# Optimization experiments

Hardware: AMD Instinct MI355X
Metric: run time of the kernel (lower is better)

The kernel has to match this reference:

```python
import jax, jax.numpy as jnp
import numpy as np

B, S, D, H = 2, 2048, 1024, 16
DK = D // H


def setup_inputs() -> dict:
    key = jax.random.key(0)
    ks = jax.random.split(key, 7)
    x = jax.random.normal(ks[0], (B, S, D), dtype=jnp.float32)
    gamma = jax.random.normal(ks[1], (D,), dtype=jnp.float32)
    mask = jax.random.randint(ks[2], (B, S), 0, 2, dtype=jnp.int32)
    w_qkv_w = jax.random.normal(ks[3], (D, 3 * D), dtype=jnp.float32) / np.sqrt(D)
    w_qkv_b = jax.random.normal(ks[4], (3 * D,), dtype=jnp.float32) * 0.02
    w_o_w = jax.random.normal(ks[5], (D, D), dtype=jnp.float32) / np.sqrt(D)
    w_o_b = jax.random.normal(ks[6], (D,), dtype=jnp.float32) * 0.02
    return {"x": x, "gamma": gamma, "mask": mask, "w_qkv_w": w_qkv_w,
            "w_qkv_b": w_qkv_b, "w_o_w": w_o_w, "w_o_b": w_o_b}


def reference(x, gamma, mask, w_qkv_w, w_qkv_b, w_o_w, w_o_b):
    b, s, d = x.shape
    # QKV projection, then per-head interleaved chunk (matches torch view+chunk)
    qkv = x @ w_qkv_w + w_qkv_b                      # [B,S,3D]
    qkv = qkv.reshape(b, s, H, 3 * DK).transpose(0, 2, 1, 3)  # [B,H,S,3*dk]
    q, k, v = jnp.split(qkv, 3, axis=-1)             # each [B,H,S,dk]
    scale = 1.0 / np.sqrt(DK).astype(np.float32)
    scores = jnp.einsum('bhqd,bhkd->bhqk', q, k) * scale  # [B,H,S,S]
    m = mask[:, None, None, :]                       # 2D mask -> [B,1,1,S]
    scores = jnp.where(m == 0, -jnp.inf, scores)
    attn = jax.nn.softmax(scores, axis=-1)           # dropout p=0.0 -> identity
    out = jnp.einsum('bhqk,bhkd->bhqd', attn, v)     # [B,H,S,dk]
    out = out.transpose(0, 2, 1, 3).reshape(b, s, d) # [B,S,D]
    out = out @ w_o_w + w_o_b
    return (gamma + 1.0) * out
```

## Files before the change

kernel.cpp:

```cpp
#include <hip/hip_runtime.h>
#include <hip/hip_bf16.h>


using bf16 = __hip_bfloat16;
typedef __attribute__((ext_vector_type(8))) short bf16x8;
typedef __attribute__((ext_vector_type(4))) float f32x4;

#define QSCALE 0.18033688011112042f

static __device__ __forceinline__ f32x4 mfma_bf16(bf16x8 a, bf16x8 b, f32x4 c) {
    return __builtin_amdgcn_mfma_f32_16x16x32_bf16(a, b, c, 0, 0, 0);
}

static __device__ __forceinline__ void gld_lds16(const void* g, void* s) {
    __builtin_amdgcn_global_load_lds(
        (const __attribute__((address_space(1))) unsigned int*)g,
        (__attribute__((address_space(3))) unsigned int*)s,
        16, 0, 0);
}

static __device__ __forceinline__ unsigned int pk_bf16(float lo, float hi) {
    unsigned int ul = __builtin_bit_cast(unsigned int, lo) + 0x8000u;
    unsigned int uh = __builtin_bit_cast(unsigned int, hi) + 0x8000u;
    return __builtin_amdgcn_perm(uh, ul, 0x07060302u);
}

__global__ void prep_kernel(const float* __restrict__ x, bf16* __restrict__ xb,
                            const float* __restrict__ wqkv, bf16* __restrict__ wqkvT,
                            const float* __restrict__ wo, bf16* __restrict__ woT) {
    __shared__ float tile[32][33];
    int blk = blockIdx.x;
    if (blk < 4096) {
        int i = blk * 256 + threadIdx.x;
        float4 f = reinterpret_cast<const float4*>(x)[i];
        xb[4*i+0] = __float2bfloat16(f.x);
        xb[4*i+1] = __float2bfloat16(f.y);
        xb[4*i+2] = __float2bfloat16(f.z);
        xb[4*i+3] = __float2bfloat16(f.w);
        return;
    }
    int xo = threadIdx.x & 31, yo = threadIdx.x >> 5;
    if (blk < 7168) {
        int idx = blk - 4096;
        int c0 = (idx % 96) * 32, r0 = (idx / 96) * 32;
#pragma unroll
        for (int i = 0; i < 32; i += 8)
            tile[yo + i][xo] = wqkv[(size_t)(r0 + yo + i) * 3072 + c0 + xo];
        __syncthreads();
#pragma unroll
        for (int i = 0; i < 32; i += 8) {
            int c = c0 + yo + i;
            int hh = c / 192, rem = c - hh * 192;
            int which = rem >> 6, dk = rem & 63;
            int rowp = which * 1024 + hh * 64 + dk;
            float sc = (which == 0) ? QSCALE : 1.0f;
            wqkvT[(size_t)rowp * 1024 + r0 + xo] = __float2bfloat16(tile[xo][yo + i] * sc);
        }
    } else {
        int idx = blk - 7168;
        int c0 = (idx & 31) * 32, r0 = (idx >> 5) * 32;
#pragma unroll
        for (int i = 0; i < 32; i += 8)
            tile[yo + i][xo] = wo[(size_t)(r0 + yo + i) * 1024 + c0 + xo];
        __syncthreads();
#pragma unroll
        for (int i = 0; i < 32; i += 8)
            woT[(size_t)(c0 + yo + i) * 1024 + r0 + xo] = __float2bfloat16(tile[xo][yo + i]);
    }
}

__global__ void transpose_v_kernel(const bf16* __restrict__ in, bf16* __restrict__ out) {
    __shared__ bf16 t[64][72];
    const int bh = blockIdx.y, s0 = blockIdx.x * 64;
    const int r = threadIdx.x >> 2, c16 = (threadIdx.x & 3) * 16;
    const uint4* src = (const uint4*)(in + ((size_t)bh * 2048 + s0 + r) * 64 + c16);
    uint4 a0 = src[0], a1 = src[1];
    *(uint4*)&t[r][c16] = a0;
    *(uint4*)&t[r][c16 + 8] = a1;
    __syncthreads();
    bf16 tmp[16];
#pragma unroll
    for (int ii = 0; ii < 16; ++ii) {
        int i = c16 + ii;
        int a = i >> 5, rem = i & 31, q = rem >> 3, jj = rem & 7;
        int sp = a * 32 + q * 4 + (jj < 4 ? jj : 16 + jj - 4);
        tmp[ii] = t[sp][r];
    }
    uint4* dst = (uint4*)(out + ((size_t)bh * 64 + r) * 2048 + s0 + c16);
    dst[0] = ((uint4*)tmp)[0];
    dst[1] = ((uint4*)tmp)[1];
}

template <int EPI, int TM, int MINW>
__global__ __launch_bounds__(256, MINW)
void gemm_bt_kernel(const bf16* __restrict__ A, const bf16* __restrict__ Bt,
                    int M, int N, int K,
                    const float* __restrict__ bias, const float* __restrict__ gamma,
                    bf16* __restrict__ Qout, bf16* __restrict__ Kout, bf16* __restrict__ Vout,
                    float* __restrict__ Cout) {
    constexpr int MI = TM / 32;
    constexpr int CA = TM / 32;
    __shared__ __align__(16) bf16 As[TM * 64];
    __shared__ __align__(16) bf16 Bs[128 * 64];

    const int tid  = threadIdx.x;
    const int wave = tid >> 6, lane = tid & 63;
    const int quad = lane >> 4, l16 = lane & 15;
    const int wr = wave >> 1, wc = wave & 1;
    const int bm = blockIdx.y, bn = blockIdx.x;

    f32x4 acc[MI][4] = {};

    const int crow = lane >> 3;
    const int sblk = (lane & 7) ^ (crow & 7);
    const bf16* gA[CA]; const bf16* gB[4]; bf16* lA[CA]; bf16* lB[4];
#pragma unroll
    for (int c = 0; c < CA; ++c) {
        int ch = wave * CA + c;
        gA[c] = A + (size_t)(bm * TM + ch * 8 + crow) * K + sblk * 8;
        lA[c] = As + ch * 512 + lane * 8;
    }
#pragma unroll
    for (int c = 0; c < 4; ++c) {
        int ch = wave * 4 + c;
        gB[c] = Bt + (size_t)(bn * 128 + ch * 8 + crow) * K + sblk * 8;
        lB[c] = Bs + ch * 512 + lane * 8;
    }
    const int xr = l16 & 7;

    for (int k0 = 0; k0 < K; k0 += 64) {
#pragma unroll
        for (int c = 0; c < CA; ++c) gld_lds16(gA[c] + k0, lA[c]);
#pragma unroll
        for (int c = 0; c < 4; ++c) gld_lds16(gB[c] + k0, lB[c]);
        __syncthreads();
#pragma unroll
        for (int ks = 0; ks < 2; ++ks) {
            bf16x8 af[MI], bfr[4];
#pragma unroll
            for (int mi = 0; mi < MI; ++mi)
                af[mi] = *(const bf16x8*)(As + (wr * (TM/2) + mi * 16 + l16) * 64 + ((4 * ks + quad) ^ xr) * 8);
#pragma unroll
            for (int ni = 0; ni < 4; ++ni)
                bfr[ni] = *(const bf16x8*)(Bs + (wc * 64 + ni * 16 + l16) * 64 + ((4 * ks + quad) ^ xr) * 8);
#pragma unroll
            for (int mi = 0; mi < MI; ++mi)
#pragma unroll
                for (int ni = 0; ni < 4; ++ni)
                    acc[mi][ni] = mfma_bf16(af[mi], bfr[ni], acc[mi][ni]);
        }
        __syncthreads();
    }

#pragma unroll
    for (int mi = 0; mi < MI; ++mi) {
#pragma unroll
        for (int ni = 0; ni < 4; ++ni) {
            int col = bn * 128 + wc * 64 + ni * 16 + l16;
            if (EPI == 0) {
                int which = col >> 10, hh = (col >> 6) & 15, dk = col & 63;
                float bsc = (which == 0) ? QSCALE : 1.0f;
                float bv = bias[hh * 192 + which * 64 + dk] * bsc;
                bf16* dst = (which == 0) ? Qout : ((which == 1) ? Kout : Vout);
#pragma unroll
                for (int r = 0; r < 4; ++r) {
                    int row = bm * TM + wr * (TM/2) + mi * 16 + quad * 4 + r;
                    int b = row >> 11, s = row & 2047;
                    dst[(((size_t)b * 16 + hh) * 2048 + s) * 64 + dk] =
                        __float2bfloat16(acc[mi][ni][r] + bv);
                }
            } else {
                float g1 = gamma[col] + 1.0f, bv = bias[col];
#pragma unroll
                for (int r = 0; r < 4; ++r) {
                    int row = bm * TM + wr * (TM/2) + mi * 16 + quad * 4 + r;
                    Cout[(size_t)row * N + col] = g1 * (acc[mi][ni][r] + bv);
                }
            }
        }
    }
}

__global__ __launch_bounds__(256, 2)
void attn_kernel(const bf16* __restrict__ Qb, const bf16* __restrict__ Kb,
                 const bf16* __restrict__ Vtp, const int* __restrict__ mask,
                 bf16* __restrict__ Aout) {
    __shared__ __align__(16) unsigned char smem[66560];
    bf16* KsB = (bf16*)smem;
    bf16* VsB = (bf16*)(smem + 32768);
    float* BiasB = (float*)(smem + 65536);

    const int bh = blockIdx.y;
    const int b = bh >> 4, h = bh & 15;
    const int q0 = blockIdx.x * 128;
    const int tid = threadIdx.x;
    const int wave = tid >> 6, lane = tid & 63;
    const int quad = lane >> 4, l16 = lane & 15;
    const int xr = l16 & 7;
    const int qw = wave & 1, kh = wave >> 1;

    bf16x8 aq[4][2];
#pragma unroll
    for (int m = 0; m < 4; ++m) {
        const bf16* qp = Qb + ((size_t)bh * 2048 + q0 + qw * 64 + m * 16 + l16) * 64;
        aq[m][0] = *(const bf16x8*)(qp + quad * 8);
        aq[m][1] = *(const bf16x8*)(qp + 32 + quad * 8);
    }

    bf16x8 ones;
#pragma unroll
    for (int j = 0; j < 8; ++j) ones[j] = (short)0x3F80;

    f32x4 O[4][4] = {};
    f32x4 Lacc[4] = {};

    const int r8 = lane >> 3, b8 = lane & 7;
    const int srcb = b8 ^ r8;
    const bf16* gK = Kb  + ((size_t)bh * 2048 + kh * 1024 + qw * 8 + r8) * 64 + srcb * 8;
    const bf16* gV = Vtp + ((size_t)bh * 64 + qw * 8 + r8) * 2048 + kh * 1024 + srcb * 8;
    bf16* lK[2][4]; bf16* lV[2][4];
#pragma unroll
    for (int p = 0; p < 2; ++p)
#pragma unroll
        for (int c = 0; c < 4; ++c) {
            lK[p][c] = KsB + (kh * 2 + p) * 4096 + c * 1024 + qw * 512 + lane * 8;
            lV[p][c] = VsB + (kh * 2 + p) * 4096 + c * 1024 + qw * 512 + lane * 8;
        }

    int mreg = 0;
#pragma unroll
    for (int c = 0; c < 4; ++c) {
        gld_lds16(gK + c * 1024, lK[0][c]);
        gld_lds16(gV + (size_t)c * 32768, lV[0][c]);
    }
    if (qw == 0) {
        BiasB[(kh * 2) * 64 + lane] = mask[b * 2048 + kh * 1024 + lane] ? -24.0f : -1e30f;
        mreg = mask[b * 2048 + kh * 1024 + 64 + lane];
    }

    for (int kt = 0; kt < 16; ++kt) {
        __syncthreads();
        const int cur = kt & 1, nxt = cur ^ 1;

        if (kt + 1 < 16) {
#pragma unroll
            for (int c = 0; c < 4; ++c) {
                gld_lds16(gK + (size_t)(kt + 1) * 4096 + c * 1024, lK[nxt][c]);
                gld_lds16(gV + (kt + 1) * 64 + (size_t)c * 32768, lV[nxt][c]);
            }
            if (qw == 0) BiasB[(kh * 2 + nxt) * 64 + lane] = mreg ? -24.0f : -1e30f;
        }
        if (kt + 2 < 16 && qw == 0) mreg = mask[b * 2048 + kh * 1024 + (kt + 2) * 64 + lane];

        const bf16* Ksc = KsB + (kh * 2 + cur) * 4096;
        const bf16* Vsc = VsB + (kh * 2 + cur) * 4096;
        const float* Bic = BiasB + (kh * 2 + cur) * 64;

        f32x4 bias4[4];
        bf16x8 bk[4][2];
#pragma unroll
        for (int kt4 = 0; kt4 < 4; ++kt4) {
            bias4[kt4] = *(const f32x4*)(Bic + kt4 * 16 + quad * 4);
            const bf16* kp = Ksc + (kt4 * 16 + l16) * 64;
            bk[kt4][0] = *(const bf16x8*)(kp + (quad ^ xr) * 8);
            bk[kt4][1] = *(const bf16x8*)(kp + ((quad + 4) ^ xr) * 8);
        }
        bf16x8 bv8[2][4];
#pragma unroll
        for (int a = 0; a < 2; ++a)
#pragma unroll
            for (int nt = 0; nt < 4; ++nt)
                bv8[a][nt] = *(const bf16x8*)(Vsc + (nt * 16 + l16) * 64 + ((a * 4 + quad) ^ xr) * 8);

#pragma unroll
        for (int m = 0; m < 4; ++m) {
            f32x4 sv[4];
#pragma unroll
            for (int kt4 = 0; kt4 < 4; ++kt4) {
                f32x4 c = {0.f, 0.f, 0.f, 0.f};
                c = mfma_bf16(bk[kt4][0], aq[m][0], c);
                c = mfma_bf16(bk[kt4][1], aq[m][1], c);
                sv[kt4] = c;
            }
            float p[4][4];
#pragma unroll
            for (int kt4 = 0; kt4 < 4; ++kt4)
#pragma unroll
                for (int r = 0; r < 4; ++r)
                    p[kt4][r] = __builtin_amdgcn_exp2f(sv[kt4][r] + bias4[kt4][r]);

#pragma unroll
            for (int a = 0; a < 2; ++a) {
                uint4 uv;
                uv.x = pk_bf16(p[2*a][0],   p[2*a][1]);
                uv.y = pk_bf16(p[2*a][2],   p[2*a][3]);
                uv.z = pk_bf16(p[2*a+1][0], p[2*a+1][1]);
                uv.w = pk_bf16(p[2*a+1][2], p[2*a+1][3]);
                bf16x8 pa = __builtin_bit_cast(bf16x8, uv);
                Lacc[m] = mfma_bf16(pa, ones, Lacc[m]);
#pragma unroll
                for (int nt = 0; nt < 4; ++nt)
                    O[m][nt] = mfma_bf16(pa, bv8[a][nt], O[m][nt]);
            }
        }
    }

    __syncthreads();
    float* mg = (float*)smem;
    float* mp = mg + (qw * 64 + lane) * 81;
    if (kh == 1) {
#pragma unroll
        for (int m = 0; m < 4; ++m) {
#pragma unroll
            for (int nt = 0; nt < 4; ++nt)
#pragma unroll
                for (int r = 0; r < 4; ++r) mp[m * 16 + nt * 4 + r] = O[m][nt][r];
#pragma unroll
            for (int r = 0; r < 4; ++r) mp[64 + m * 4 + r] = Lacc[m][r];
        }
    }
    __syncthreads();
    if (kh == 0) {
#pragma unroll
        for (int m = 0; m < 4; ++m) {
#pragma unroll
            for (int nt = 0; nt < 4; ++nt)
#pragma unroll
                for (int r = 0; r < 4; ++r) O[m][nt][r] += mp[m * 16 + nt * 4 + r];
#pragma unroll
            for (int r = 0; r < 4; ++r) Lacc[m][r] += mp[64 + m * 4 + r];
        }
#pragma unroll
        for (int m = 0; m < 4; ++m) {
            float inv[4];
#pragma unroll
            for (int r = 0; r < 4; ++r) inv[r] = __builtin_amdgcn_rcpf(Lacc[m][r]);
#pragma unroll
            for (int nt = 0; nt < 4; ++nt) {
#pragma unroll
                for (int r = 0; r < 4; ++r) {
                    int row = q0 + qw * 64 + m * 16 + quad * 4 + r;
                    Aout[((size_t)b * 2048 + row) * 1024 + h * 64 + nt * 16 + l16] =
                        __float2bfloat16(O[m][nt][r] * inv[r]);
                }
            }
        }
    }
}

extern "C" void kernel_launch(void* const* d_in, const int* in_sizes, int n_in,
                              void* d_out, int out_size, void* d_ws, size_t ws_size,
                              hipStream_t stream) {
    const float* x     = (const float*)d_in[0];
    const float* gamma = (const float*)d_in[1];
    const int*   mask  = (const int*)d_in[2];
    const float* wqkv  = (const float*)d_in[3];
    const float* bqkv  = (const float*)d_in[4];
    const float* wo    = (const float*)d_in[5];
    const float* bo    = (const float*)d_in[6];
    float* out = (float*)d_out;

    char* ws = (char*)d_ws;
    const size_t MB = 1u << 20;
    bf16* xb    = (bf16*)(ws);
    bf16* wqkvT = (bf16*)(ws + 8 * MB);
    bf16* woT   = (bf16*)(ws + 14 * MB);
    bf16* Qb    = (bf16*)(ws + 16 * MB);
    bf16* Kb    = (bf16*)(ws + 24 * MB);
    bf16* Vt    = (bf16*)(ws + 32 * MB);
    bf16* Vtmp  = (bf16*)(ws + 40 * MB);
    bf16* attn  = (bf16*)(ws + 40 * MB);

    prep_kernel<<<8192, 256, 0, stream>>>(x, xb, wqkv, wqkvT, wo, woT);

    gemm_bt_kernel<0, 128, 3><<<dim3(24, 32), 256, 0, stream>>>(
        xb, wqkvT, 4096, 3072, 1024, bqkv, nullptr, Qb, Kb, Vtmp, nullptr);

    transpose_v_kernel<<<dim3(32, 32), 256, 0, stream>>>(Vtmp, Vt);

    attn_kernel<<<dim3(16, 32), 256, 0, stream>>>(Qb, Kb, Vt, mask, attn);

    gemm_bt_kernel<1, 64, 4><<<dim3(8, 64), 256, 0, stream>>>(
        attn, woT, 4096, 1024, 1024, bo, gamma, nullptr, nullptr, nullptr, out);
}
```

Measured before the change: 200.1 us.

## Fuse V transpose into QKV GEMM epilogue and drop attention key-split

The QKV GEMM epilogue for V column blocks now stages results in shared memory and writes V already transposed in the permuted layout attention expects, removing the separate transpose kernel and its round trip through memory. The attention kernel is also reworked from 4 waves splitting keys into two halves to 2 waves that each walk all keys. This drops the cross-wave shared-memory reduction at the end, at the cost of halving threads per block and doubling the serial key loop length. The launch bounds change to 128 threads with one block per SM hint, which may reduce latency hiding.

```diff
diff --git a/kernel.cpp b/kernel.cpp
--- a/kernel.cpp
+++ b/kernel.cpp
@@ -69,28 +69,6 @@
     }
 }
 
-__global__ void transpose_v_kernel(const bf16* __restrict__ in, bf16* __restrict__ out) {
-    __shared__ bf16 t[64][72];
-    const int bh = blockIdx.y, s0 = blockIdx.x * 64;
-    const int r = threadIdx.x >> 2, c16 = (threadIdx.x & 3) * 16;
-    const uint4* src = (const uint4*)(in + ((size_t)bh * 2048 + s0 + r) * 64 + c16);
-    uint4 a0 = src[0], a1 = src[1];
-    *(uint4*)&t[r][c16] = a0;
-    *(uint4*)&t[r][c16 + 8] = a1;
-    __syncthreads();
-    bf16 tmp[16];
-#pragma unroll
-    for (int ii = 0; ii < 16; ++ii) {
-        int i = c16 + ii;
-        int a = i >> 5, rem = i & 31, q = rem >> 3, jj = rem & 7;
-        int sp = a * 32 + q * 4 + (jj < 4 ? jj : 16 + jj - 4);
-        tmp[ii] = t[sp][r];
-    }
-    uint4* dst = (uint4*)(out + ((size_t)bh * 64 + r) * 2048 + s0 + c16);
-    dst[0] = ((uint4*)tmp)[0];
-    dst[1] = ((uint4*)tmp)[1];
-}
-
 template <int EPI, int TM, int MINW>
 __global__ __launch_bounds__(256, MINW)
 void gemm_bt_kernel(const bf16* __restrict__ A, const bf16* __restrict__ Bt,
@@ -100,8 +78,9 @@
                     float* __restrict__ Cout) {
     constexpr int MI = TM / 32;
     constexpr int CA = TM / 32;
-    __shared__ __align__(16) bf16 As[TM * 64];
-    __shared__ __align__(16) bf16 Bs[128 * 64];
+    __shared__ __align__(16) bf16 smem[TM * 64 + 128 * 64];
+    bf16* As = smem;
+    bf16* Bs = smem + TM * 64;
 
     const int tid  = threadIdx.x;
     const int wave = tid >> 6, lane = tid & 63;
@@ -152,6 +131,41 @@
         __syncthreads();
     }
 
+    if (EPI == 0 && bn >= 16) {
+        __syncthreads();
+        uint2* Tu = (uint2*)smem;
+#pragma unroll
+        for (int mi = 0; mi < MI; ++mi) {
+#pragma unroll
+            for (int ni = 0; ni < 4; ++ni) {
+                int colL = wc * 64 + ni * 16 + l16;
+                float bv = bias[(2 * (bn - 16) + wc) * 192 + 128 + (ni * 16 + l16)];
+                uint2 pk;
+                pk.x = pk_bf16(acc[mi][ni][0] + bv, acc[mi][ni][1] + bv);
+                pk.y = pk_bf16(acc[mi][ni][2] + bv, acc[mi][ni][3] + bv);
+                int rg = wr * 16 + mi * 4 + quad;
+                Tu[colL * 32 + (rg ^ (colL & 31))] = pk;
+            }
+        }
+        __syncthreads();
+        const int sub = tid & 15, rbase = tid >> 4;
+        const int cs = sub >> 3, aa = (sub >> 2) & 1, qq = sub & 3;
+        const int g1 = cs * 16 + aa * 8 + qq;
+        const int g2 = g1 + 4;
+        const int b = bm >> 4;
+        const int s0 = (bm & 15) * 128;
+#pragma unroll
+        for (int j = 0; j < 8; ++j) {
+            int rt = rbase + 16 * j;
+            int hh = 2 * (bn - 16) + (rt >> 6), dk = rt & 63;
+            uint2 lo = Tu[rt * 32 + (g1 ^ (rt & 31))];
+            uint2 hi = Tu[rt * 32 + (g2 ^ (rt & 31))];
+            uint4 val; val.x = lo.x; val.y = lo.y; val.z = hi.x; val.w = hi.y;
+            *(uint4*)(Vout + (((size_t)b * 16 + hh) * 64 + dk) * 2048 + s0 + sub * 8) = val;
+        }
+        return;
+    }
+
 #pragma unroll
     for (int mi = 0; mi < MI; ++mi) {
 #pragma unroll
@@ -159,9 +173,9 @@
             int col = bn * 128 + wc * 64 + ni * 16 + l16;
             if (EPI == 0) {
                 int which = col >> 10, hh = (col >> 6) & 15, dk = col & 63;
-                float bsc = (which == 0) ? QSCALE : 1.0f;
-                float bv = bias[hh * 192 + which * 64 + dk] * bsc;
-                bf16* dst = (which == 0) ? Qout : ((which == 1) ? Kout : Vout);
+                float bv = bias[hh * 192 + which * 64 + dk];
+                if (which == 0) bv *= QSCALE;
+                bf16* dst = which ? Kout : Qout;
 #pragma unroll
                 for (int r = 0; r < 4; ++r) {
                     int row = bm * TM + wr * (TM/2) + mi * 16 + quad * 4 + r;
@@ -181,14 +195,13 @@
     }
 }
 
-__global__ __launch_bounds__(256, 2)
+__global__ __launch_bounds__(128, 1)
 void attn_kernel(const bf16* __restrict__ Qb, const bf16* __restrict__ Kb,
                  const bf16* __restrict__ Vtp, const int* __restrict__ mask,
                  bf16* __restrict__ Aout) {
-    __shared__ __align__(16) unsigned char smem[66560];
-    bf16* KsB = (bf16*)smem;
-    bf16* VsB = (bf16*)(smem + 32768);
-    float* BiasB = (float*)(smem + 65536);
+    __shared__ __align__(16) bf16 Ks[2][64 * 64];
+    __shared__ __align__(16) bf16 Vs[2][64 * 64];
+    __shared__ float Biass[2][64];
 
     const int bh = blockIdx.y;
     const int b = bh >> 4, h = bh & 15;
@@ -197,12 +210,11 @@
     const int wave = tid >> 6, lane = tid & 63;
     const int quad = lane >> 4, l16 = lane & 15;
     const int xr = l16 & 7;
-    const int qw = wave & 1, kh = wave >> 1;
 
     bf16x8 aq[4][2];
 #pragma unroll
     for (int m = 0; m < 4; ++m) {
-        const bf16* qp = Qb + ((size_t)bh * 2048 + q0 + qw * 64 + m * 16 + l16) * 64;
+        const bf16* qp = Qb + ((size_t)bh * 2048 + q0 + wave * 64 + m * 16 + l16) * 64;
         aq[m][0] = *(const bf16x8*)(qp + quad * 8);
         aq[m][1] = *(const bf16x8*)(qp + 32 + quad * 8);
     }
@@ -216,15 +228,15 @@
 
     const int r8 = lane >> 3, b8 = lane & 7;
     const int srcb = b8 ^ r8;
-    const bf16* gK = Kb  + ((size_t)bh * 2048 + kh * 1024 + qw * 8 + r8) * 64 + srcb * 8;
-    const bf16* gV = Vtp + ((size_t)bh * 64 + qw * 8 + r8) * 2048 + kh * 1024 + srcb * 8;
+    const bf16* gK = Kb  + ((size_t)bh * 2048 + wave * 8 + r8) * 64 + srcb * 8;
+    const bf16* gV = Vtp + ((size_t)bh * 64 + wave * 8 + r8) * 2048 + srcb * 8;
     bf16* lK[2][4]; bf16* lV[2][4];
 #pragma unroll
     for (int p = 0; p < 2; ++p)
 #pragma unroll
         for (int c = 0; c < 4; ++c) {
-            lK[p][c] = KsB + (kh * 2 + p) * 4096 + c * 1024 + qw * 512 + lane * 8;
-            lV[p][c] = VsB + (kh * 2 + p) * 4096 + c * 1024 + qw * 512 + lane * 8;
+            lK[p][c] = Ks[p] + c * 1024 + wave * 512 + lane * 8;
+            lV[p][c] = Vs[p] + c * 1024 + wave * 512 + lane * 8;
         }
 
     int mreg = 0;
@@ -233,35 +245,31 @@
         gld_lds16(gK + c * 1024, lK[0][c]);
         gld_lds16(gV + (size_t)c * 32768, lV[0][c]);
     }
-    if (qw == 0) {
-        BiasB[(kh * 2) * 64 + lane] = mask[b * 2048 + kh * 1024 + lane] ? -24.0f : -1e30f;
-        mreg = mask[b * 2048 + kh * 1024 + 64 + lane];
-    }
-
-    for (int kt = 0; kt < 16; ++kt) {
+    if (tid < 64) {
+        Biass[0][tid] = mask[b * 2048 + tid] ? -24.0f : -1e30f;
+        mreg = mask[b * 2048 + 64 + tid];
+    }
+
+    for (int kt = 0; kt < 32; ++kt) {
         __syncthreads();
         const int cur = kt & 1, nxt = cur ^ 1;
 
-        if (kt + 1 < 16) {
+        if (kt + 1 < 32) {
 #pragma unroll
             for (int c = 0; c < 4; ++c) {
                 gld_lds16(gK + (size_t)(kt + 1) * 4096 + c * 1024, lK[nxt][c]);
                 gld_lds16(gV + (kt + 1) * 64 + (size_t)c * 32768, lV[nxt][c]);
             }
-            if (qw == 0) BiasB[(kh * 2 + nxt) * 64 + lane] = mreg ? -24.0f : -1e30f;
-        }
-        if (kt + 2 < 16 && qw == 0) mreg = mask[b * 2048 + kh * 1024 + (kt + 2) * 64 + lane];
-
-        const bf16* Ksc = KsB + (kh * 2 + cur) * 4096;
-        const bf16* Vsc = VsB + (kh * 2 + cur) * 4096;
-        const float* Bic = BiasB + (kh * 2 + cur) * 64;
+            if (tid < 64) Biass[nxt][tid] = mreg ? -24.0f : -1e30f;
+        }
+        if (kt + 2 < 32 && tid < 64) mreg = mask[b * 2048 + (kt + 2) * 64 + tid];
 
         f32x4 bias4[4];
         bf16x8 bk[4][2];
 #pragma unroll
         for (int kt4 = 0; kt4 < 4; ++kt4) {
-            bias4[kt4] = *(const f32x4*)(Bic + kt4 * 16 + quad * 4);
-            const bf16* kp = Ksc + (kt4 * 16 + l16) * 64;
+            bias4[kt4] = *(const f32x4*)(&Biass[cur][0] + kt4 * 16 + quad * 4);
+            const bf16* kp = Ks[cur] + (kt4 * 16 + l16) * 64;
             bk[kt4][0] = *(const bf16x8*)(kp + (quad ^ xr) * 8);
             bk[kt4][1] = *(const bf16x8*)(kp + ((quad + 4) ^ xr) * 8);
         }
@@ -270,7 +278,7 @@
         for (int a = 0; a < 2; ++a)
 #pragma unroll
             for (int nt = 0; nt < 4; ++nt)
-                bv8[a][nt] = *(const bf16x8*)(Vsc + (nt * 16 + l16) * 64 + ((a * 4 + quad) ^ xr) * 8);
+                bv8[a][nt] = *(const bf16x8*)(Vs[cur] + (nt * 16 + l16) * 64 + ((a * 4 + quad) ^ xr) * 8);
 
 #pragma unroll
         for (int m = 0; m < 4; ++m) {
@@ -305,44 +313,18 @@
         }
     }
 
-    __syncthreads();
-    float* mg = (float*)smem;
-    float* mp = mg + (qw * 64 + lane) * 81;
-    if (kh == 1) {
-#pragma unroll
-        for (int m = 0; m < 4; ++m) {
-#pragma unroll
-            for (int nt = 0; nt < 4; ++nt)
-#pragma unroll
-                for (int r = 0; r < 4; ++r) mp[m * 16 + nt * 4 + r] = O[m][nt][r];
-#pragma unroll
-            for (int r = 0; r < 4; ++r) mp[64 + m * 4 + r] = Lacc[m][r];
-        }
-    }
-    __syncthreads();
-    if (kh == 0) {
-#pragma unroll
-        for (int m = 0; m < 4; ++m) {
-#pragma unroll
-            for (int nt = 0; nt < 4; ++nt)
-#pragma unroll
-                for (int r = 0; r < 4; ++r) O[m][nt][r] += mp[m * 16 + nt * 4 + r];
-#pragma unroll
-            for (int r = 0; r < 4; ++r) Lacc[m][r] += mp[64 + m * 4 + r];
-        }
-#pragma unroll
-        for (int m = 0; m < 4; ++m) {
-            float inv[4];
-#pragma unroll
-            for (int r = 0; r < 4; ++r) inv[r] = __builtin_amdgcn_rcpf(Lacc[m][r]);
-#pragma unroll
-            for (int nt = 0; nt < 4; ++nt) {
-#pragma unroll
-                for (int r = 0; r < 4; ++r) {
-                    int row = q0 + qw * 64 + m * 16 + quad * 4 + r;
-                    Aout[((size_t)b * 2048 + row) * 1024 + h * 64 + nt * 16 + l16] =
-                        __float2bfloat16(O[m][nt][r] * inv[r]);
-                }
+#pragma unroll
+    for (int m = 0; m < 4; ++m) {
+        float inv[4];
+#pragma unroll
+        for (int r = 0; r < 4; ++r) inv[r] = __builtin_amdgcn_rcpf(Lacc[m][r]);
+#pragma unroll
+        for (int nt = 0; nt < 4; ++nt) {
+#pragma unroll
+            for (int r = 0; r < 4; ++r) {
+                int row = q0 + wave * 64 + m * 16 + quad * 4 + r;
+                Aout[((size_t)b * 2048 + row) * 1024 + h * 64 + nt * 16 + l16] =
+                    __float2bfloat16(O[m][nt][r] * inv[r]);
             }
         }
     }
@@ -368,17 +350,14 @@
     bf16* Qb    = (bf16*)(ws + 16 * MB);
     bf16* Kb    = (bf16*)(ws + 24 * MB);
     bf16* Vt    = (bf16*)(ws + 32 * MB);
-    bf16* Vtmp  = (bf16*)(ws + 40 * MB);
     bf16* attn  = (bf16*)(ws + 40 * MB);
 
     prep_kernel<<<8192, 256, 0, stream>>>(x, xb, wqkv, wqkvT, wo, woT);
 
     gemm_bt_kernel<0, 128, 3><<<dim3(24, 32), 256, 0, stream>>>(
-        xb, wqkvT, 4096, 3072, 1024, bqkv, nullptr, Qb, Kb, Vtmp, nullptr);
-
-    transpose_v_kernel<<<dim3(32, 32), 256, 0, stream>>>(Vtmp, Vt);
-
-    attn_kernel<<<dim3(16, 32), 256, 0, stream>>>(Qb, Kb, Vt, mask, attn);
+        xb, wqkvT, 4096, 3072, 1024, bqkv, nullptr, Qb, Kb, Vt, nullptr);
+
+    attn_kernel<<<dim3(16, 32), 128, 0, stream>>>(Qb, Kb, Vt, mask, attn);
 
     gemm_bt_kernel<1, 64, 4><<<dim3(8, 64), 256, 0, stream>>>(
         attn, woT, 4096, 1024, 1024, bo, gamma, nullptr, nullptr, nullptr, out);
```

Result: faster. 191.9 us (-4.1%).
